# Kernel tuning notes

Hardware: AMD Instinct MI355X
Metric: run time of the kernel (lower is better)

The kernel has to match this reference:

```python
import jax, jax.numpy as jnp
import numpy as np

B, NQ, NK, C = 16, 8, 4096, 256
H = W = 64
HEADS = 8
CI = 128          # embedding_dim // attention_downsample_rate
HD = CI // HEADS  # per-head dim
EPS = float(np.finfo(np.float32).tiny)


def _gumbel_topk(scores, noise, n):
    # iterative gumbel-softmax top-k relaxation with straight-through hard k-hot
    g = scores + noise
    khot = jnp.zeros_like(g)
    onehot = jnp.zeros_like(g)
    for _ in range(n):
        g = g + jnp.log(jnp.maximum(1.0 - onehot, EPS))
        onehot = jax.nn.softmax(g, axis=-1)
        khot = khot + onehot
    _, ind = jax.lax.top_k(khot, n)
    rows = jnp.arange(khot.shape[0])[:, None]
    hard = jnp.zeros_like(khot).at[rows, ind].set(1.0)
    ret = hard - jax.lax.stop_gradient(khot) + khot  # == hard numerically
    return ret, jnp.sort(ind, axis=1)  # sorted idx = row-major order of boolean-mask select


def _sample_points(pe, content, ret, idx):
    # pe [H,W,C], content [b,H,W,C], ret [b,HW] k-hot, idx [b,k] sorted
    b = ret.shape[0]
    m = ret.reshape(b, H, W, 1)
    pe_m = (pe[None] * m).reshape(b, H * W, -1)
    c_m = (content * m).reshape(b, H * W, -1)
    take = lambda a: jnp.take_along_axis(a, idx[:, :, None], axis=1)
    return take(pe_m), take(c_m)


def _mlp(x, W1, b1, W2, b2, W3, b3):
    x = jax.nn.relu(x @ W1 + b1)
    x = jax.nn.relu(x @ W2 + b2)
    return x @ W3 + b3


def _forward(queries, keys, query_pe, key_pe, guiding_embedding, gumbel_p, gumbel_n,
             static_uncertain, static_refined, Wq, bq, Wk, bk, Wv, bv, Wo, bo,
             uW1, ub1, uW2, ub2, uW3, ub3, rW1, rb1, rW2, rb2, rW3, rb3,
             pe_gauss, point_pos, point_neg, n_sample_points):
    b = queries.shape[0]
    g = guiding_embedding.reshape(b, C, H * W).transpose(0, 2, 1)  # [b, HW, C]
    g = g * keys  # elementwise gating -> new guiding embedding

    # cross attention token -> image (internal dim CI, HEADS heads)
    def split_heads(x, Wx, bx):
        return (x @ Wx + bx).reshape(b, -1, HEADS, HD).transpose(0, 2, 1, 3)
    qh = split_heads(queries + query_pe, Wq, bq)
    kh = split_heads(g + key_pe, Wk, bk)
    vh = split_heads(g, Wv, bv)
    attn = jax.nn.softmax(jnp.einsum('bhqd,bhkd->bhqk', qh, kh) / np.float32(np.sqrt(HD)), axis=-1)
    out = jnp.einsum('bhqk,bhkd->bhqd', attn, vh).transpose(0, 2, 1, 3).reshape(b, -1, CI)
    queries = out @ Wo + bo  # [b, NQ, C]

    q1 = queries[:, 1, :]
    unc_tok = _mlp(jnp.concatenate([jnp.broadcast_to(static_uncertain, (b, C)), q1], -1),
                   uW1, ub1, uW2, ub2, uW3, ub3)
    ref_tok = _mlp(jnp.concatenate([jnp.broadcast_to(static_refined, (b, C)), q1], -1),
                   rW1, rb1, rW2, rb2, rW3, rb3)

    img = g.transpose(0, 2, 1)  # [b, C, HW]
    unc_norm = jax.nn.sigmoid(jnp.einsum('bc,bcn->bn', unc_tok, img))
    ref_mask = jnp.einsum('bc,bcn->bn', ref_tok, img)
    coarse_mask = jnp.einsum('bc,bcn->bn', q1, img)

    queries = jnp.concatenate([queries[:, 0:1], ref_tok[:, None, :], queries[:, 2:]], axis=1)

    # point-sampling reference map + gumbel-softmax top-k (training-path math)
    ref_map = unc_norm * (jax.nn.sigmoid(ref_mask) - jax.nn.sigmoid(coarse_mask))  # [b, HW]
    ret_p, idx_p = _gumbel_topk(ref_map, gumbel_p, n_sample_points)
    ret_n, idx_n = _gumbel_topk(-ref_map, gumbel_n, n_sample_points)

    # random fourier positional encoding of the 64x64 grid (SAM PositionEmbeddingRandom)
    xs = (jnp.arange(W, dtype=jnp.float32) + 0.5) / W
    ys = (jnp.arange(H, dtype=jnp.float32) + 0.5) / H
    coords = jnp.stack([jnp.tile(xs[None, :], (H, 1)), jnp.tile(ys[:, None], (1, W))], axis=-1)
    proj = ((2.0 * coords - 1.0) @ pe_gauss) * np.float32(2.0 * np.pi)  # [H, W, C//2]
    pe = jnp.concatenate([jnp.sin(proj), jnp.cos(proj)], axis=-1)       # [H, W, C]

    # F.interpolate of a 64x64 map to (64,64) is the identity here
    content = (keys + g).reshape(b, H, W, C)

    sp_pe, sp_c = _sample_points(pe, content, ret_p, idx_p)
    sn_pe, sn_c = _sample_points(pe, content, ret_n, idx_n)
    sp_pe = sp_pe + point_pos  # prompt_encoder.point_embeddings[1]
    sn_pe = sn_pe + point_neg  # prompt_encoder.point_embeddings[0]

    query_pe = jnp.concatenate([query_pe, sp_pe, sn_pe], axis=1)
    queries = jnp.concatenate([queries, sp_c, sn_c], axis=1)
    # pack (queries, query_pe) into one array for a single-output reference
    return jnp.concatenate([queries, query_pe], axis=1)  # [b, 2*(NQ+2k), C]


def setup_inputs():
    key = jax.random.key(0)
    ks = iter(jax.random.split(key, 48))
    n = lambda shape, s=1.0: jax.random.normal(next(ks), shape, jnp.float32) * s
    z = lambda shape: jnp.zeros(shape, jnp.float32)
    return {
        'queries': n((B, NQ, C)),
        'keys': n((B, NK, C)),
        'query_pe': n((B, NQ, C)),
        'key_pe': n((B, NK, C)),
        'guiding_embedding': n((B, C, H, W)),
        'gumbel_p': jax.random.gumbel(next(ks), (B, NK), jnp.float32),
        'gumbel_n': jax.random.gumbel(next(ks), (B, NK), jnp.float32),
        'static_uncertain': n((C,), 0.02),
        'static_refined': n((C,), 0.02),
        'Wq': n((C, CI), 0.02), 'bq': z((CI,)),
        'Wk': n((C, CI), 0.02), 'bk': z((CI,)),
        'Wv': n((C, CI), 0.02), 'bv': z((CI,)),
        'Wo': n((CI, C), 0.02), 'bo': z((C,)),
        'uW1': n((2 * C, C // 4), 0.05), 'ub1': z((C // 4,)),
        'uW2': n((C // 4, C // 4), 0.05), 'ub2': z((C // 4,)),
        'uW3': n((C // 4, C), 0.05), 'ub3': z((C,)),
        'rW1': n((2 * C, C // 4), 0.05), 'rb1': z((C // 4,)),
        'rW2': n((C // 4, C // 4), 0.05), 'rb2': z((C // 4,)),
        'rW3': n((C // 4, C), 0.05), 'rb3': z((C,)),
        'pe_gauss': n((2, C // 2)),
        'point_pos': n((C,), 0.02),
        'point_neg': n((C,), 0.02),
        'n_sample_points': 4,
    }


def reference(queries, keys, query_pe, key_pe, guiding_embedding, gumbel_p, gumbel_n,
              static_uncertain, static_refined, Wq, bq, Wk, bk, Wv, bv, Wo, bo,
              uW1, ub1, uW2, ub2, uW3, ub3, rW1, rb1, rW2, rb2, rW3, rb3,
              pe_gauss, point_pos, point_neg, n_sample_points):
    return _forward(queries, keys, query_pe, key_pe, guiding_embedding, gumbel_p, gumbel_n,
                    static_uncertain, static_refined, Wq, bq, Wk, bk, Wv, bv, Wo, bo,
                    uW1, ub1, uW2, ub2, uW3, ub3, rW1, rb1, rW2, rb2, rW3, rb3,
                    pe_gauss, point_pos, point_neg, n_sample_points)
```

## Files before the change

### kernel.cpp

```cpp
#include <hip/hip_runtime.h>

#define BB 16
#define NQn 8
#define NK 4096
#define CC 256
#define NHEADS 8
#define CIn 128
#define HDn 16
#define NHQ 64
#define EPS_TINY 1.17549435e-38f

constexpr size_t OFF_QK   = 0;
constexpr size_t OFF_QBK  = OFF_QK  + (size_t)BB*CC*NHQ;
constexpr size_t OFF_SC   = OFF_QBK + (size_t)BB*NHQ;
constexpr size_t OFF_MP   = OFF_SC  + (size_t)BB*NK*NHQ;
constexpr size_t OFF_SP   = OFF_MP  + (size_t)BB*16*NHQ;
constexpr size_t OFF_M    = OFF_SP  + (size_t)BB*16*NHQ;
constexpr size_t OFF_RS   = OFF_M   + (size_t)BB*NHQ;
constexpr size_t OFF_AVP  = OFF_RS  + (size_t)BB*NHQ;
constexpr size_t OFF_QATT = OFF_AVP + (size_t)BB*16*NHQ*CC;
constexpr size_t OFF_UNC  = OFF_QATT+ (size_t)BB*NQn*CC;
constexpr size_t OFF_REFT = OFF_UNC + (size_t)BB*CC;
constexpr size_t OFF_RMAP = OFF_REFT+ (size_t)BB*CC;
constexpr size_t OFF_IDX  = OFF_RMAP+ (size_t)BB*NK;
constexpr size_t OFF_RV   = OFF_IDX + 128;
constexpr size_t OFF_G    = OFF_RV  + 128;

__global__ __launch_bounds__(256) void k1_qside(
    const float* __restrict__ queries, const float* __restrict__ query_pe,
    const float* __restrict__ Wq, const float* __restrict__ bq,
    const float* __restrict__ Wk, const float* __restrict__ bk,
    float* __restrict__ ws)
{
  int b = blockIdx.x >> 3, q = blockIdx.x & 7, t = threadIdx.x;
  __shared__ float x[CC];
  __shared__ float qh[CIn];
  x[t] = queries[(b*NQn+q)*CC + t] + query_pe[(b*NQn+q)*CC + t];
  __syncthreads();
  if (t < CIn) {
    float a = bq[t];
    for (int c = 0; c < CC; ++c) a += x[c]*Wq[c*CIn + t];
    qh[t] = a * 0.25f;
  }
  __syncthreads();
  float* Qk = ws + OFF_QK;
  #pragma unroll
  for (int h = 0; h < NHEADS; ++h) {
    float a = 0.f;
    #pragma unroll
    for (int d = 0; d < HDn; ++d) a += qh[h*HDn+d] * Wk[t*CIn + h*HDn + d];
    Qk[((size_t)b*CC + t)*NHQ + h*NQn + q] = a;
  }
  if (t < NHEADS) {
    float a = 0.f;
    #pragma unroll
    for (int d = 0; d < HDn; ++d) a += qh[t*HDn+d] * bk[t*HDn+d];
    (ws + OFF_QBK)[b*NHQ + t*NQn + q] = a;
  }
}

__global__ __launch_bounds__(256) void k2_scores(
    const float* __restrict__ keys, const float* __restrict__ key_pe,
    const float* __restrict__ guiding, float* __restrict__ ws)
{
  int b = blockIdx.y, n0 = blockIdx.x * 64, t = threadIdx.x;
  __shared__ __align__(16) float Xs[64][68];
  __shared__ __align__(16) float Qs[64][64];
  __shared__ float Gt[64][65];
  const float* Qk = ws + OFF_QK;
  float* G = ws + OFF_G;
  int tx = t & 15, ty = t >> 4;
  int c4 = (t & 15)*4, rowg = t >> 4;
  int lane = t & 63, grp = t >> 6;
  float acc[4][4] = {};
  for (int c0 = 0; c0 < CC; c0 += 64) {
    __syncthreads();
    #pragma unroll
    for (int cc = 0; cc < 16; ++cc) {
      int c = grp*16 + cc;
      Gt[c][lane] = guiding[((size_t)b*CC + c0 + c)*NK + n0 + lane];
    }
    #pragma unroll
    for (int i = 0; i < 16; ++i) {
      int l = i*256 + t;
      Qs[l >> 6][l & 63] = Qk[((size_t)b*CC + c0 + (l>>6))*NHQ + (l & 63)];
    }
    __syncthreads();
    #pragma unroll
    for (int p = 0; p < 4; ++p) {
      int row = p*16 + rowg;
      size_t base = ((size_t)b*NK + n0 + row)*CC + c0 + c4;
      float4 kv = *(const float4*)&keys[base];
      float4 pv = *(const float4*)&key_pe[base];
      float4 g4;
      g4.x = kv.x * Gt[c4+0][row];
      g4.y = kv.y * Gt[c4+1][row];
      g4.z = kv.z * Gt[c4+2][row];
      g4.w = kv.w * Gt[c4+3][row];
      *(float4*)&G[base] = g4;
      float4 o; o.x = g4.x+pv.x; o.y = g4.y+pv.y; o.z = g4.z+pv.z; o.w = g4.w+pv.w;
      *(float4*)&Xs[row][c4] = o;
    }
    __syncthreads();
    #pragma unroll 4
    for (int cb = 0; cb < 16; ++cb) {
      float4 xf[4], qf[4];
      #pragma unroll
      for (int i = 0; i < 4; ++i) xf[i] = *(const float4*)&Xs[4*ty+i][4*cb];
      #pragma unroll
      for (int u = 0; u < 4; ++u) qf[u] = *(const float4*)&Qs[4*cb+u][4*tx];
      #pragma unroll
      for (int u = 0; u < 4; ++u) {
        float xu[4] = { ((const float*)&xf[0])[u], ((const float*)&xf[1])[u],
                        ((const float*)&xf[2])[u], ((const float*)&xf[3])[u] };
        float qu[4] = { qf[u].x, qf[u].y, qf[u].z, qf[u].w };
        #pragma unroll
        for (int i = 0; i < 4; ++i)
          #pragma unroll
          for (int j = 0; j < 4; ++j) acc[i][j] += xu[i]*qu[j];
      }
    }
  }
  const float* qbk = ws + OFF_QBK + (size_t)b*NHQ;
  float qb[4] = {qbk[4*tx], qbk[4*tx+1], qbk[4*tx+2], qbk[4*tx+3]};
  float* sc = ws + OFF_SC + ((size_t)b*NK + n0)*NHQ;
  #pragma unroll
  for (int i = 0; i < 4; ++i) {
    float4 o;
    o.x = acc[i][0]+qb[0]; o.y = acc[i][1]+qb[1]; o.z = acc[i][2]+qb[2]; o.w = acc[i][3]+qb[3];
    *(float4*)&sc[(4*ty + i)*NHQ + 4*tx] = o;
  }
}

__global__ __launch_bounds__(256) void k3a_stats(float* __restrict__ ws)
{
  int b = blockIdx.y, sb = blockIdx.x, t = threadIdx.x;
  int hq = t & 63, r = t >> 6;
  const float* sc = ws + OFF_SC + ((size_t)b*NK + sb*256)*NHQ;
  float m = -INFINITY, s = 0.f;
  for (int i = 0; i < 64; ++i) {
    float v = sc[(r + 4*i)*NHQ + hq];
    if (v > m) { s = s*expf(m - v) + 1.f; m = v; } else { s += expf(v - m); }
  }
  __shared__ float rm[256], rs[256];
  rm[t] = m; rs[t] = s;
  __syncthreads();
  if (t < 64) {
    float m0=rm[t], m1=rm[t+64], m2=rm[t+128], m3=rm[t+192];
    float mm = fmaxf(fmaxf(m0,m1), fmaxf(m2,m3));
    float ss = rs[t]*expf(m0-mm) + rs[t+64]*expf(m1-mm) + rs[t+128]*expf(m2-mm) + rs[t+192]*expf(m3-mm);
    (ws + OFF_MP)[(b*16 + sb)*NHQ + t] = mm;
    (ws + OFF_SP)[(b*16 + sb)*NHQ + t] = ss;
  }
}

__global__ __launch_bounds__(64) void k3b_combine(float* __restrict__ ws)
{
  int b = blockIdx.x, hq = threadIdx.x;
  const float* mp = ws + OFF_MP + (size_t)b*16*NHQ;
  const float* sp = ws + OFF_SP + (size_t)b*16*NHQ;
  float m = -INFINITY;
  #pragma unroll
  for (int i = 0; i < 16; ++i) m = fmaxf(m, mp[i*NHQ+hq]);
  float s = 0.f;
  #pragma unroll
  for (int i = 0; i < 16; ++i) s += sp[i*NHQ+hq]*expf(mp[i*NHQ+hq]-m);
  (ws+OFF_M)[b*NHQ+hq] = m;
  (ws+OFF_RS)[b*NHQ+hq] = 1.0f/s;
}

__global__ __launch_bounds__(512) void k4_av(float* __restrict__ ws)
{
  int b = blockIdx.y, kb = blockIdx.x, t = threadIdx.x;
  int k0 = kb * 256;
  __shared__ __align__(16) float gld[32][260];
  __shared__ __align__(16) float wld[32][64];
  __shared__ float mv[64], rv[64];
  if (t < 64) { mv[t] = (ws+OFF_M)[b*NHQ+t]; rv[t] = (ws+OFF_RS)[b*NHQ+t]; }
  int hq0 = (t & 7) * 8, c0 = (t >> 3) * 4;
  float accf[8][4] = {};
  const float* sc = ws + OFF_SC;
  const float* G  = ws + OFF_G;
  for (int kk = 0; kk < 256; kk += 32) {
    __syncthreads();
    #pragma unroll
    for (int p = 0; p < 4; ++p) {
      int row = p*8 + (t>>6);
      *(float4*)&gld[row][(t&63)*4] =
        *(const float4*)&G[((size_t)b*NK + k0+kk+row)*CC + (t&63)*4];
    }
    #pragma unroll
    for (int i = 0; i < 4; ++i) {
      int l = i*512 + t; int k = l >> 6, hq = l & 63;
      float v = sc[((size_t)b*NK + k0+kk+k)*NHQ + hq];
      wld[k][hq] = expf(v - mv[hq]) * rv[hq];
    }
    __syncthreads();
    #pragma unroll 2
    for (int k = 0; k < 32; ++k) {
      float4 w0 = *(const float4*)&wld[k][hq0];
      float4 w1 = *(const float4*)&wld[k][hq0+4];
      float4 gv = *(const float4*)&gld[k][c0];
      float wq[8] = {w0.x,w0.y,w0.z,w0.w, w1.x,w1.y,w1.z,w1.w};
      float gq[4] = {gv.x,gv.y,gv.z,gv.w};
      #pragma unroll
      for (int i = 0; i < 8; ++i)
        #pragma unroll
        for (int j = 0; j < 4; ++j) accf[i][j] += wq[i]*gq[j];
    }
  }
  float* avp = ws + OFF_AVP + (((size_t)b*16 + kb)*NHQ)*CC;
  #pragma unroll
  for (int i = 0; i < 8; ++i) {
    float4 o;
    o.x = accf[i][0]; o.y = accf[i][1]; o.z = accf[i][2]; o.w = accf[i][3];
    *(float4*)&avp[(size_t)(hq0 + i)*CC + c0] = o;
  }
}

__global__ __launch_bounds__(256) void k56_attout(
    const float* __restrict__ Wv, const float* __restrict__ bv,
    const float* __restrict__ Wo, const float* __restrict__ bo,
    float* __restrict__ ws)
{
  int b = blockIdx.x >> 3, q = blockIdx.x & 7, t = threadIdx.x;
  __shared__ float avs[NHEADS][CC];
  __shared__ float outv[CIn];
  const float* avp = ws + OFF_AVP;
  #pragma unroll
  for (int h = 0; h < NHEADS; ++h) {
    int hq = h*NQn + q;
    float a = 0.f;
    #pragma unroll 4
    for (int kb = 0; kb < 16; ++kb)
      a += avp[(((size_t)b*16 + kb)*NHQ + hq)*CC + t];
    avs[h][t] = a;
  }
  __syncthreads();
  if (t < CIn) {
    int h = t >> 4;
    float a = bv[t];
    for (int c = 0; c < CC; ++c) a += avs[h][c]*Wv[c*CIn + t];
    outv[t] = a;
  }
  __syncthreads();
  float a = bo[t];
  for (int ci = 0; ci < CIn; ++ci) a += outv[ci]*Wo[ci*CC + t];
  (ws+OFF_QATT)[((size_t)b*NQn + q)*CC + t] = a;
}

__global__ __launch_bounds__(256) void k7_mlps(
    const float* __restrict__ su, const float* __restrict__ sr,
    const float* __restrict__ uW1, const float* __restrict__ ub1,
    const float* __restrict__ uW2, const float* __restrict__ ub2,
    const float* __restrict__ uW3, const float* __restrict__ ub3,
    const float* __restrict__ rW1, const float* __restrict__ rb1,
    const float* __restrict__ rW2, const float* __restrict__ rb2,
    const float* __restrict__ rW3, const float* __restrict__ rb3,
    float* __restrict__ ws)
{
  int b = blockIdx.x, t = threadIdx.x;
  __shared__ float xs[768];
  __shared__ float h1[2][64], h2[2][64];
  xs[t] = su[t];
  xs[256+t] = (ws+OFF_QATT)[((size_t)b*NQn + 1)*CC + t];
  xs[512+t] = sr[t];
  __syncthreads();
  if (t < 128) {
    int which = t >> 6, o = t & 63;
    const float* W1 = which ? rW1 : uW1;
    const float* b1 = which ? rb1 : ub1;
    int base = which ? 512 : 0;
    float a = b1[o];
    for (int i = 0; i < 256; ++i) a += xs[base+i]*W1[i*64 + o];
    for (int i = 0; i < 256; ++i) a += xs[256+i]*W1[(256+i)*64 + o];
    h1[which][o] = fmaxf(a, 0.f);
  }
  __syncthreads();
  if (t < 128) {
    int which = t >> 6, o = t & 63;
    const float* W2 = which ? rW2 : uW2;
    const float* b2 = which ? rb2 : ub2;
    float a = b2[o];
    #pragma unroll 8
    for (int i = 0; i < 64; ++i) a += h1[which][i]*W2[i*64+o];
    h2[which][o] = fmaxf(a, 0.f);
  }
  __syncthreads();
  {
    float a = ub3[t];
    #pragma unroll 8
    for (int i = 0; i < 64; ++i) a += h2[0][i]*uW3[i*CC + t];
    (ws+OFF_UNC)[b*CC + t] = a;
    float a2 = rb3[t];
    #pragma unroll 8
    for (int i = 0; i < 64; ++i) a2 += h2[1][i]*rW3[i*CC + t];
    (ws+OFF_REFT)[b*CC + t] = a2;
  }
}

__global__ __launch_bounds__(256) void k8_masks(float* __restrict__ ws)
{
  int b = blockIdx.y, t = threadIdx.x;
  int wave = t >> 6, lane = t & 63;
  __shared__ float q1s[CC], us[CC], rts[CC];
  q1s[t] = (ws+OFF_QATT)[((size_t)b*NQn+1)*CC + t];
  us[t]  = (ws+OFF_UNC)[b*CC + t];
  rts[t] = (ws+OFF_REFT)[b*CC + t];
  __syncthreads();
  float q1v[4], usv[4], rtv[4];
  #pragma unroll
  for (int u = 0; u < 4; ++u) {
    q1v[u] = q1s[lane*4+u]; usv[u] = us[lane*4+u]; rtv[u] = rts[lane*4+u];
  }
  const float* G = ws + OFF_G;
  float* rmap = ws + OFF_RMAP + (size_t)b*NK;
  int n_base = blockIdx.x*64 + wave*16;
  for (int r = 0; r < 16; ++r) {
    int n = n_base + r;
    float4 gv = *(const float4*)&G[((size_t)b*NK + n)*CC + lane*4];
    float aq = gv.x*q1v[0] + gv.y*q1v[1] + gv.z*q1v[2] + gv.w*q1v[3];
    float au = gv.x*usv[0] + gv.y*usv[1] + gv.z*usv[2] + gv.w*usv[3];
    float ar = gv.x*rtv[0] + gv.y*rtv[1] + gv.z*rtv[2] + gv.w*rtv[3];
    #pragma unroll
    for (int s = 1; s < 64; s <<= 1) {
      aq += __shfl_xor(aq, s, 64);
      au += __shfl_xor(au, s, 64);
      ar += __shfl_xor(ar, s, 64);
    }
    if (lane == 0) {
      float un = 1.f/(1.f+expf(-au));
      rmap[n] = un * (1.f/(1.f+expf(-ar)) - 1.f/(1.f+expf(-aq)));
    }
  }
}

__global__ __launch_bounds__(256) void k9_gumbel(
    const float* __restrict__ gp, const float* __restrict__ gn,
    float* __restrict__ ws)
{
  int sign = blockIdx.x, b = blockIdx.y, t = threadIdx.x;
  const float* noise = sign ? gn : gp;
  const float* rmap = ws + OFF_RMAP + (size_t)b*NK;
  float g[16], kh[16], oh[16];
  #pragma unroll
  for (int i = 0; i < 16; ++i) {
    int n = i*256 + t;
    float scv = rmap[n];
    if (sign) scv = -scv;
    g[i] = scv + noise[(size_t)b*NK + n];
    kh[i] = 0.f; oh[i] = 0.f;
  }
  __shared__ float rv[256];
  __shared__ int ri[256];
  for (int it = 0; it < 4; ++it) {
    if (it > 0) {
      #pragma unroll
      for (int i = 0; i < 16; ++i) g[i] += logf(fmaxf(1.f - oh[i], EPS_TINY));
    }
    float m = g[0];
    #pragma unroll
    for (int i = 1; i < 16; ++i) m = fmaxf(m, g[i]);
    rv[t] = m; __syncthreads();
    for (int s = 128; s > 0; s >>= 1) { if (t < s) rv[t] = fmaxf(rv[t], rv[t+s]); __syncthreads(); }
    m = rv[0]; __syncthreads();
    float e[16], ls = 0.f;
    #pragma unroll
    for (int i = 0; i < 16; ++i) { e[i] = expf(g[i]-m); ls += e[i]; }
    rv[t] = ls; __syncthreads();
    for (int s = 128; s > 0; s >>= 1) { if (t < s) rv[t] += rv[t+s]; __syncthreads(); }
    float ssum = rv[0]; __syncthreads();
    #pragma unroll
    for (int i = 0; i < 16; ++i) { oh[i] = e[i]/ssum; kh[i] += oh[i]; }
  }
  __shared__ int selI[4]; __shared__ float selR[4];
  for (int j = 0; j < 4; ++j) {
    float bvv = kh[0]; int bii = t;
    #pragma unroll
    for (int i = 1; i < 16; ++i) {
      if (kh[i] > bvv) { bvv = kh[i]; bii = i*256 + t; }
    }
    rv[t] = bvv; ri[t] = bii; __syncthreads();
    for (int s = 128; s > 0; s >>= 1) {
      if (t < s) {
        float v2 = rv[t+s]; int i2 = ri[t+s];
        if (v2 > rv[t] || (v2 == rv[t] && i2 < ri[t])) { rv[t] = v2; ri[t] = i2; }
      }
      __syncthreads();
    }
    int bidx = ri[0]; float bkh = rv[0];
    if (t == 0) { selI[j] = bidx; selR[j] = (1.f - bkh) + bkh; }
    if (t == (bidx & 255)) {
      int slot = bidx >> 8;
      #pragma unroll
      for (int i = 0; i < 16; ++i) if (i == slot) kh[i] = -1.f;
    }
    __syncthreads();
  }
  if (t == 0) {
    int id[4]; float rr[4];
    #pragma unroll
    for (int j = 0; j < 4; ++j) { id[j] = selI[j]; rr[j] = selR[j]; }
    for (int a = 0; a < 3; ++a)
      for (int c2 = a+1; c2 < 4; ++c2)
        if (id[c2] < id[a]) { int ti=id[a]; id[a]=id[c2]; id[c2]=ti; float tr=rr[a]; rr[a]=rr[c2]; rr[c2]=tr; }
    int* iout = (int*)(ws + OFF_IDX);
    float* rout = ws + OFF_RV;
    for (int j = 0; j < 4; ++j) {
      iout[(sign*BB + b)*4 + j] = id[j];
      rout[(sign*BB + b)*4 + j] = rr[j];
    }
  }
}

__global__ __launch_bounds__(256) void k10_out(
    const float* __restrict__ keys, const float* __restrict__ query_pe,
    const float* __restrict__ point_pos, const float* __restrict__ point_neg,
    const float* __restrict__ pe_gauss,
    float* __restrict__ ws, float* __restrict__ out)
{
  int b = blockIdx.y, r = blockIdx.x, t = threadIdx.x;
  const float* G = ws + OFF_G;
  float val;
  if (r < 8) {
    val = (r == 1) ? (ws+OFF_REFT)[b*CC + t]
                   : (ws+OFF_QATT)[((size_t)b*NQn + r)*CC + t];
  } else if (r < 16) {
    int j = r - 8; int sign = j >> 2; int jj = j & 3;
    int idx = ((const int*)(ws+OFF_IDX))[(sign*BB + b)*4 + jj];
    float rvv = (ws+OFF_RV)[(sign*BB + b)*4 + jj];
    float kv = keys[((size_t)b*NK + idx)*CC + t];
    float gv = G[((size_t)b*NK + idx)*CC + t];
    val = (kv + gv) * rvv;
  } else if (r < 24) {
    val = query_pe[((size_t)b*NQn + (r-16))*CC + t];
  } else {
    int j = r - 24; int sign = j >> 2; int jj = j & 3;
    int idx = ((const int*)(ws+OFF_IDX))[(sign*BB + b)*4 + jj];
    float rvv = (ws+OFF_RV)[(sign*BB + b)*4 + jj];
    const float* point = sign ? point_neg : point_pos;
    int h = idx >> 6, w = idx & 63;
    float x = (w + 0.5f)/64.f, y = (h + 0.5f)/64.f;
    int jf = (t < 128) ? t : (t - 128);
    float proj = ((2.f*x - 1.f)*pe_gauss[jf] + (2.f*y - 1.f)*pe_gauss[128 + jf]) * 6.28318530717958647692f;
    float sv = (t < 128) ? sinf(proj) : cosf(proj);
    val = sv*rvv + point[t];
  }
  out[((size_t)b*32 + r)*CC + t] = val;
}

extern "C" void kernel_launch(void* const* d_in, const int* in_sizes, int n_in,
                              void* d_out, int out_size, void* d_ws, size_t ws_size,
                              hipStream_t stream)
{
  const float* queries   = (const float*)d_in[0];
  const float* keys      = (const float*)d_in[1];
  const float* query_pe  = (const float*)d_in[2];
  const float* key_pe    = (const float*)d_in[3];
  const float* guiding   = (const float*)d_in[4];
  const float* gumbel_p  = (const float*)d_in[5];
  const float* gumbel_n  = (const float*)d_in[6];
  const float* s_unc     = (const float*)d_in[7];
  const float* s_ref     = (const float*)d_in[8];
  const float* Wq  = (const float*)d_in[9];   const float* bq  = (const float*)d_in[10];
  const float* Wk  = (const float*)d_in[11];  const float* bk  = (const float*)d_in[12];
  const float* Wv  = (const float*)d_in[13];  const float* bv  = (const float*)d_in[14];
  const float* Wo  = (const float*)d_in[15];  const float* bo  = (const float*)d_in[16];
  const float* uW1 = (const float*)d_in[17];  const float* ub1 = (const float*)d_in[18];
  const float* uW2 = (const float*)d_in[19];  const float* ub2 = (const float*)d_in[20];
  const float* uW3 = (const float*)d_in[21];  const float* ub3 = (const float*)d_in[22];
  const float* rW1 = (const float*)d_in[23];  const float* rb1 = (const float*)d_in[24];
  const float* rW2 = (const float*)d_in[25];  const float* rb2 = (const float*)d_in[26];
  const float* rW3 = (const float*)d_in[27];  const float* rb3 = (const float*)d_in[28];
  const float* pe_gauss  = (const float*)d_in[29];
  const float* point_pos = (const float*)d_in[30];
  const float* point_neg = (const float*)d_in[31];
  float* ws = (float*)d_ws;
  float* out = (float*)d_out;

  k1_qside  <<<dim3(BB*NQn),  256, 0, stream>>>(queries, query_pe, Wq, bq, Wk, bk, ws);
  k2_scores <<<dim3(64, BB),  256, 0, stream>>>(keys, key_pe, guiding, ws);
  k3a_stats <<<dim3(16, BB),  256, 0, stream>>>(ws);
  k3b_combine<<<dim3(BB),      64, 0, stream>>>(ws);
  k4_av     <<<dim3(16, BB),  512, 0, stream>>>(ws);
  k56_attout<<<dim3(BB*NQn),  256, 0, stream>>>(Wv, bv, Wo, bo, ws);
  k7_mlps   <<<dim3(BB),      256, 0, stream>>>(s_unc, s_ref, uW1, ub1, uW2, ub2, uW3, ub3,
                                                rW1, rb1, rW2, rb2, rW3, rb3, ws);
  k8_masks  <<<dim3(64, BB),  256, 0, stream>>>(ws);
  k9_gumbel <<<dim3(2, BB),   256, 0, stream>>>(gumbel_p, gumbel_n, ws);
  k10_out   <<<dim3(32, BB),  256, 0, stream>>>(keys, query_pe, point_pos, point_neg,
                                                pe_gauss, ws, out);
}
```

Baseline: 249.5 us.

## Prefetch next tiles into registers and use wave-shuffle reductions in gumbel

In the score kernel and the attention-times-value kernel, the next tile's global loads are issued into registers before the current tile's compute. This lets memory latency overlap the FMA loop, and the barrier placement is rearranged to suit. The gumbel top-k kernel swaps its shared-memory tree reductions for 64-lane shuffle reductions plus a small cross-wave combine, which cuts the number of barriers. In exchange, the prefetch buffers raise register pressure and may lower occupancy, and the dynamic register-array index in the top-k kernel could spill to scratch.

```diff
diff --git a/kernel.cpp b/kernel.cpp
--- a/kernel.cpp
+++ b/kernel.cpp
@@ -70,28 +70,42 @@
   const float* Qk = ws + OFF_QK;
   float* G = ws + OFF_G;
   int tx = t & 15, ty = t >> 4;
-  int c4 = (t & 15)*4, rowg = t >> 4;
+  int c4 = tx*4, rowg = ty;
   int lane = t & 63, grp = t >> 6;
   float acc[4][4] = {};
+
+  float gpref[16];
+  float4 kpref[4], ppref[4];
+  float qpref[16];
+  #pragma unroll
+  for (int cc = 0; cc < 16; ++cc)
+    gpref[cc] = guiding[((size_t)b*CC + grp*16+cc)*NK + n0 + lane];
+  #pragma unroll
+  for (int p = 0; p < 4; ++p) {
+    size_t base = ((size_t)b*NK + n0 + p*16+rowg)*CC + c4;
+    kpref[p] = *(const float4*)&keys[base];
+    ppref[p] = *(const float4*)&key_pe[base];
+  }
+  #pragma unroll
+  for (int i = 0; i < 16; ++i) {
+    int l = i*256 + t;
+    qpref[i] = Qk[((size_t)b*CC + (l>>6))*NHQ + (l & 63)];
+  }
+
   for (int c0 = 0; c0 < CC; c0 += 64) {
-    __syncthreads();
-    #pragma unroll
-    for (int cc = 0; cc < 16; ++cc) {
-      int c = grp*16 + cc;
-      Gt[c][lane] = guiding[((size_t)b*CC + c0 + c)*NK + n0 + lane];
-    }
+    #pragma unroll
+    for (int cc = 0; cc < 16; ++cc) Gt[grp*16+cc][lane] = gpref[cc];
+    __syncthreads();
     #pragma unroll
     for (int i = 0; i < 16; ++i) {
       int l = i*256 + t;
-      Qs[l >> 6][l & 63] = Qk[((size_t)b*CC + c0 + (l>>6))*NHQ + (l & 63)];
-    }
-    __syncthreads();
+      Qs[l >> 6][l & 63] = qpref[i];
+    }
     #pragma unroll
     for (int p = 0; p < 4; ++p) {
       int row = p*16 + rowg;
       size_t base = ((size_t)b*NK + n0 + row)*CC + c0 + c4;
-      float4 kv = *(const float4*)&keys[base];
-      float4 pv = *(const float4*)&key_pe[base];
+      float4 kv = kpref[p], pv = ppref[p];
       float4 g4;
       g4.x = kv.x * Gt[c4+0][row];
       g4.y = kv.y * Gt[c4+1][row];
@@ -102,6 +116,23 @@
       *(float4*)&Xs[row][c4] = o;
     }
     __syncthreads();
+    if (c0 + 64 < CC) {
+      int c1 = c0 + 64;
+      #pragma unroll
+      for (int cc = 0; cc < 16; ++cc)
+        gpref[cc] = guiding[((size_t)b*CC + c1 + grp*16+cc)*NK + n0 + lane];
+      #pragma unroll
+      for (int p = 0; p < 4; ++p) {
+        size_t base = ((size_t)b*NK + n0 + p*16+rowg)*CC + c1 + c4;
+        kpref[p] = *(const float4*)&keys[base];
+        ppref[p] = *(const float4*)&key_pe[base];
+      }
+      #pragma unroll
+      for (int i = 0; i < 16; ++i) {
+        int l = i*256 + t;
+        qpref[i] = Qk[((size_t)b*CC + c1 + (l>>6))*NHQ + (l & 63)];
+      }
+    }
     #pragma unroll 4
     for (int cb = 0; cb < 16; ++cb) {
       float4 xf[4], qf[4];
@@ -181,21 +212,42 @@
   float accf[8][4] = {};
   const float* sc = ws + OFF_SC;
   const float* G  = ws + OFF_G;
+  float4 gpref[4]; float spref[4];
+  #pragma unroll
+  for (int p = 0; p < 4; ++p) {
+    int row = p*8 + (t>>6);
+    gpref[p] = *(const float4*)&G[((size_t)b*NK + k0 + row)*CC + (t&63)*4];
+  }
+  #pragma unroll
+  for (int i = 0; i < 4; ++i) {
+    int l = i*512 + t;
+    spref[i] = sc[((size_t)b*NK + k0 + (l>>6))*NHQ + (l&63)];
+  }
+  __syncthreads();
   for (int kk = 0; kk < 256; kk += 32) {
-    __syncthreads();
     #pragma unroll
     for (int p = 0; p < 4; ++p) {
       int row = p*8 + (t>>6);
-      *(float4*)&gld[row][(t&63)*4] =
-        *(const float4*)&G[((size_t)b*NK + k0+kk+row)*CC + (t&63)*4];
+      *(float4*)&gld[row][(t&63)*4] = gpref[p];
     }
     #pragma unroll
     for (int i = 0; i < 4; ++i) {
       int l = i*512 + t; int k = l >> 6, hq = l & 63;
-      float v = sc[((size_t)b*NK + k0+kk+k)*NHQ + hq];
-      wld[k][hq] = expf(v - mv[hq]) * rv[hq];
-    }
-    __syncthreads();
+      wld[k][hq] = expf(spref[i] - mv[hq]) * rv[hq];
+    }
+    __syncthreads();
+    if (kk + 32 < 256) {
+      #pragma unroll
+      for (int p = 0; p < 4; ++p) {
+        int row = p*8 + (t>>6);
+        gpref[p] = *(const float4*)&G[((size_t)b*NK + k0 + kk+32 + row)*CC + (t&63)*4];
+      }
+      #pragma unroll
+      for (int i = 0; i < 4; ++i) {
+        int l = i*512 + t;
+        spref[i] = sc[((size_t)b*NK + k0 + kk+32 + (l>>6))*NHQ + (l&63)];
+      }
+    }
     #pragma unroll 2
     for (int k = 0; k < 32; ++k) {
       float4 w0 = *(const float4*)&wld[k][hq0];
@@ -208,6 +260,7 @@
         #pragma unroll
         for (int j = 0; j < 4; ++j) accf[i][j] += wq[i]*gq[j];
     }
+    __syncthreads();
   }
   float* avp = ws + OFF_AVP + (((size_t)b*16 + kb)*NHQ)*CC;
   #pragma unroll
@@ -340,6 +393,7 @@
     float* __restrict__ ws)
 {
   int sign = blockIdx.x, b = blockIdx.y, t = threadIdx.x;
+  int wave = t >> 6, lane = t & 63;
   const float* noise = sign ? gn : gp;
   const float* rmap = ws + OFF_RMAP + (size_t)b*NK;
   float g[16], kh[16], oh[16];
@@ -351,8 +405,9 @@
     g[i] = scv + noise[(size_t)b*NK + n];
     kh[i] = 0.f; oh[i] = 0.f;
   }
-  __shared__ float rv[256];
-  __shared__ int ri[256];
+  __shared__ float wred[8];
+  __shared__ float selV[16];
+  __shared__ int   selIdx[16];
   for (int it = 0; it < 4; ++it) {
     if (it > 0) {
       #pragma unroll
@@ -361,46 +416,47 @@
     float m = g[0];
     #pragma unroll
     for (int i = 1; i < 16; ++i) m = fmaxf(m, g[i]);
-    rv[t] = m; __syncthreads();
-    for (int s = 128; s > 0; s >>= 1) { if (t < s) rv[t] = fmaxf(rv[t], rv[t+s]); __syncthreads(); }
-    m = rv[0]; __syncthreads();
+    #pragma unroll
+    for (int s = 1; s < 64; s <<= 1) m = fmaxf(m, __shfl_xor(m, s, 64));
+    if (lane == 0) wred[wave] = m;
+    __syncthreads();
+    m = fmaxf(fmaxf(wred[0], wred[1]), fmaxf(wred[2], wred[3]));
     float e[16], ls = 0.f;
     #pragma unroll
     for (int i = 0; i < 16; ++i) { e[i] = expf(g[i]-m); ls += e[i]; }
-    rv[t] = ls; __syncthreads();
-    for (int s = 128; s > 0; s >>= 1) { if (t < s) rv[t] += rv[t+s]; __syncthreads(); }
-    float ssum = rv[0]; __syncthreads();
+    #pragma unroll
+    for (int s = 1; s < 64; s <<= 1) ls += __shfl_xor(ls, s, 64);
+    if (lane == 0) wred[4+wave] = ls;
+    __syncthreads();
+    float ssum = wred[4]+wred[5]+wred[6]+wred[7];
     #pragma unroll
     for (int i = 0; i < 16; ++i) { oh[i] = e[i]/ssum; kh[i] += oh[i]; }
   }
-  __shared__ int selI[4]; __shared__ float selR[4];
+  int id[4]; float rr[4];
   for (int j = 0; j < 4; ++j) {
-    float bvv = kh[0]; int bii = t;
+    float bv = kh[0]; int bi = t;
     #pragma unroll
     for (int i = 1; i < 16; ++i) {
-      if (kh[i] > bvv) { bvv = kh[i]; bii = i*256 + t; }
-    }
-    rv[t] = bvv; ri[t] = bii; __syncthreads();
-    for (int s = 128; s > 0; s >>= 1) {
-      if (t < s) {
-        float v2 = rv[t+s]; int i2 = ri[t+s];
-        if (v2 > rv[t] || (v2 == rv[t] && i2 < ri[t])) { rv[t] = v2; ri[t] = i2; }
-      }
-      __syncthreads();
-    }
-    int bidx = ri[0]; float bkh = rv[0];
-    if (t == 0) { selI[j] = bidx; selR[j] = (1.f - bkh) + bkh; }
-    if (t == (bidx & 255)) {
-      int slot = bidx >> 8;
-      #pragma unroll
-      for (int i = 0; i < 16; ++i) if (i == slot) kh[i] = -1.f;
-    }
-    __syncthreads();
+      if (kh[i] > bv) { bv = kh[i]; bi = i*256 + t; }
+    }
+    #pragma unroll
+    for (int s = 1; s < 64; s <<= 1) {
+      float ov = __shfl_xor(bv, s, 64);
+      int   oi = __shfl_xor(bi, s, 64);
+      if (ov > bv || (ov == bv && oi < bi)) { bv = ov; bi = oi; }
+    }
+    if (lane == 0) { selV[j*4+wave] = bv; selIdx[j*4+wave] = bi; }
+    __syncthreads();
+    bv = selV[j*4]; bi = selIdx[j*4];
+    #pragma unroll
+    for (int w = 1; w < 4; ++w) {
+      float ov = selV[j*4+w]; int oi = selIdx[j*4+w];
+      if (ov > bv || (ov == bv && oi < bi)) { bv = ov; bi = oi; }
+    }
+    id[j] = bi; rr[j] = (1.f - bv) + bv;
+    if ((bi & 255) == t) kh[bi >> 8] = -1.f;
   }
   if (t == 0) {
-    int id[4]; float rr[4];
-    #pragma unroll
-    for (int j = 0; j < 4; ++j) { id[j] = selI[j]; rr[j] = selR[j]; }
     for (int a = 0; a < 3; ++a)
       for (int c2 = a+1; c2 < 4; ++c2)
         if (id[c2] < id[a]) { int ti=id[a]; id[a]=id[c2]; id[c2]=ti; float tr=rr[a]; rr[a]=rr[c2]; rr[c2]=tr; }
```

New measurement: 243.3 us. 2.5% less time.
